# Performance work log

Measured on AMD Instinct MI355X. Metric: run time of the kernel, lower is better.

## Reference

```python
import jax, jax.numpy as jnp
import numpy as np

# Config (matches init_kwargs)
B, C, H, W = 32, 128, 12, 1200   # z: (B, in_dim, H, W)
DIN = C * H                       # 1536
FIX = 768                         # get_multiple(DIN // 2, 6)
OV = 4                            # overlap
G = 6                             # num_vqs
D = OV * FIX // G                 # 512 per-group embedding size (all equal)
K = 1024                          # codebook_size
COMMIT = 0.25


def setup_inputs() -> dict:
    key = jax.random.key(0)
    k1, k2, k3, k4 = jax.random.split(key, 4)
    z = jax.random.normal(k1, (B, C, H, W), dtype=jnp.float32)
    w_down = jax.random.normal(k2, (FIX, DIN), dtype=jnp.float32) * 0.02
    w_up = jax.random.normal(k3, (DIN, FIX), dtype=jnp.float32) * 0.02
    embedding = jax.random.normal(k4, (G, D, K), dtype=jnp.float32)  # per-group (embedding_size, num_embedding)
    return {"z": z, "w_down": w_down, "w_up": w_up, "embedding": embedding}


def _quantize_group(zg, emb):
    # zg: (B, T, D), emb: (D, K)
    zf = zg.reshape(-1, D)
    # squared euclidean distance: |z|^2 - 2 z@E + |E|^2 -> (N, K)
    dist = (zf * zf).sum(1, keepdims=True) - 2.0 * (zf @ emb) + (emb * emb).sum(0, keepdims=True)
    idx = jnp.argmin(dist, axis=1)            # (N,)
    q = jnp.take(emb.T, idx, axis=0).reshape(zg.shape)
    # straight-through estimator (training mode)
    zq = zg + jax.lax.stop_gradient(q - zg)
    loss = COMMIT * jnp.mean((jax.lax.stop_gradient(zq) - zg) ** 2)
    return zq, loss


def reference(z, w_down, w_up, embedding):
    # pre_process: (B,C,H,W) -> permute(0,2,3,1) -> permute(0,2,3,1) -> (B, W, C*H)
    x = jnp.transpose(z, (0, 3, 1, 2)).reshape(B, W, DIN)  # (B, W, C, H) flattened
    x = x @ w_down.T                                       # proj_down -> (B, W, FIX)
    T = W // OV
    x = x.reshape(B, T, OV * FIX)                          # (B, T, 3072)
    # split into G contiguous groups of size D along last axis -> (G, B, T, D)
    xg = jnp.transpose(x.reshape(B, T, G, D), (2, 0, 1, 3))
    zq_g, losses = jax.vmap(_quantize_group)(xg, embedding)
    vq_loss = losses.sum() / G
    # concat groups back -> (B, T, G*D)
    zq = jnp.transpose(zq_g, (1, 2, 0, 3)).reshape(B, T, G * D)
    # post_process: un-overlap, proj_up, back to (B, C, H, W)
    zq = zq.reshape(B, W, FIX)
    zq = zq @ w_up.T                                       # (B, W, DIN)
    zq = zq.reshape(B, W, C, H)
    zq = jnp.transpose(zq, (0, 3, 1, 2))                   # (B, H, W, C)
    zq = jnp.transpose(zq, (0, 3, 1, 2))                   # dim==4 -> (B, C, H, W)
    return zq, vq_loss
```

## Files before the change

kernel.cpp:

```cpp
#include <hip/hip_runtime.h>

#define BB 32
#define CC 128
#define HH 12
#define WW 1200
#define DIN 1536
#define FIXD 768
#define OVL 4
#define GG 6
#define DD 512
#define KK 1024
#define TT 300
#define NV 9600
#define MROWS 38400

#define Y_OFF     0
#define ET_OFF    29491200
#define NORM_OFF  32636928
#define BEST_OFF  32643072
#define LOSS_OFF  32758272
#define ZN_OFF    32758336
#define CNT_OFF   32873536
#define MAXN_OFF  32931136
#define LIST_OFF  32931200
#define YBF_OFF   36617600
#define EBF_OFF   51363200

#define BSWZ(c) ((c) + 4 * ((c) >> 5))

typedef __attribute__((ext_vector_type(8))) short bf16x8;
typedef __attribute__((ext_vector_type(4))) float f32x4;

static __device__ inline unsigned short f2bf(float x) {
    unsigned u = __float_as_uint(x);
    unsigned r = (u + 0x7fffu + ((u >> 16) & 1u)) >> 16;
    return (unsigned short)r;
}
static __device__ inline unsigned enc32(float s) {
    unsigned u = __float_as_uint(s);
    return (u & 0x80000000u) ? ~u : (u | 0x80000000u);
}

__global__ __launch_bounds__(256) void k_gemm_down(const float* __restrict__ z,
                                                   const float* __restrict__ w_down,
                                                   float* __restrict__ Y) {
    __shared__ float As[16][132];
    __shared__ float Bs[16][140];
    const int n0 = blockIdx.y * 128, f0 = blockIdx.x * 128;
    const int tid = threadIdx.x;
    const int arow = tid & 127;
    const int ak0 = tid >> 7;
    const int nA = n0 + arow;
    const int bA = nA / WW, wA = nA - bA * WW;
    const size_t zbase = (size_t)bA * (CC * HH * WW) + wA;
    const int bcol = tid >> 1, bq = tid & 1;
    const int bsc = BSWZ(bcol);
    const int trow = tid >> 4, tcol = tid & 15;
    const int bread = tcol * 8 + 4 * (tcol >> 2);
    float acc[8][8] = {};
    for (int kt = 0; kt < DIN; kt += 16) {
        #pragma unroll
        for (int i = 0; i < 8; i++) {
            const int kk = ak0 + i * 2;
            As[kk][arow] = z[zbase + (size_t)(kt + kk) * WW];
        }
        #pragma unroll
        for (int i = 0; i < 2; i++) {
            const int q = bq + i * 2;
            const float4 v = *(const float4*)&w_down[(size_t)(f0 + bcol) * DIN + kt + q * 4];
            Bs[q * 4 + 0][bsc] = v.x;
            Bs[q * 4 + 1][bsc] = v.y;
            Bs[q * 4 + 2][bsc] = v.z;
            Bs[q * 4 + 3][bsc] = v.w;
        }
        __syncthreads();
        #pragma unroll
        for (int k = 0; k < 16; k++) {
            float av[8], bv[8];
            *(float4*)&av[0] = *(const float4*)&As[k][trow * 8];
            *(float4*)&av[4] = *(const float4*)&As[k][trow * 8 + 4];
            *(float4*)&bv[0] = *(const float4*)&Bs[k][bread];
            *(float4*)&bv[4] = *(const float4*)&Bs[k][bread + 4];
            #pragma unroll
            for (int i = 0; i < 8; i++)
                #pragma unroll
                for (int j = 0; j < 8; j++)
                    acc[i][j] = fmaf(av[i], bv[j], acc[i][j]);
        }
        __syncthreads();
    }
    #pragma unroll
    for (int i = 0; i < 8; i++) {
        float4 o0, o1;
        o0.x = acc[i][0]; o0.y = acc[i][1]; o0.z = acc[i][2]; o0.w = acc[i][3];
        o1.x = acc[i][4]; o1.y = acc[i][5]; o1.z = acc[i][6]; o1.w = acc[i][7];
        float* yr = &Y[(size_t)(n0 + trow * 8 + i) * FIXD + f0 + tcol * 8];
        *(float4*)yr = o0;
        *(float4*)(yr + 4) = o1;
    }
}

__global__ __launch_bounds__(256) void k_transpose(const float* __restrict__ emb,
                                                   float* __restrict__ ET) {
    int i = blockIdx.x * 256 + threadIdx.x;
    if (i >= GG * KK * DD) return;
    int d = i & 511;
    int rem = i >> 9;
    int k = rem & 1023;
    int g = rem >> 10;
    ET[i] = emb[((g * DD + d) << 10) + k];
}

__global__ __launch_bounds__(64) void k_norms(const float* __restrict__ ET,
                                              float* __restrict__ norms,
                                              unsigned* __restrict__ maxnU) {
    const int code = blockIdx.x;
    const int lane = threadIdx.x;
    const float* row = ET + code * DD;
    double s = 0.0;
    #pragma unroll
    for (int r = 0; r < 8; r++) {
        float v = row[lane + r * 64];
        s += (double)v * (double)v;
    }
    #pragma unroll
    for (int off = 32; off; off >>= 1) s += __shfl_down(s, off);
    if (lane == 0) {
        const float nf = (float)s;
        norms[code] = nf;
        atomicMax(&maxnU[code >> 10], __float_as_uint(nf));
    }
}

__global__ __launch_bounds__(256) void k_ysplit(const float* __restrict__ Y,
                                                unsigned short* __restrict__ Ybf,
                                                float* __restrict__ znorm) {
    const int gv = blockIdx.x * 4 + (threadIdx.x >> 6);
    const int lane = threadIdx.x & 63;
    const int g = gv / NV, r = gv - g * NV;
    const int b = r / TT, t = r - b * TT;
    const int d0 = lane * 8;
    const int p = g * DD + d0;
    const int sg = p / FIXD, f = p - sg * FIXD;
    const float* yb = &Y[(size_t)((b * WW + t * OVL + sg) * FIXD + f)];
    const float4 y0 = *(const float4*)yb;
    const float4 y1 = *(const float4*)(yb + 4);
    unsigned short h[8];
    h[0] = f2bf(y0.x); h[1] = f2bf(y0.y); h[2] = f2bf(y0.z); h[3] = f2bf(y0.w);
    h[4] = f2bf(y1.x); h[5] = f2bf(y1.y); h[6] = f2bf(y1.z); h[7] = f2bf(y1.w);
    *(uint4*)&Ybf[(size_t)gv * DD + d0] = *(uint4*)&h[0];
    float s = 0.f;
    s = fmaf(y0.x, y0.x, s); s = fmaf(y0.y, y0.y, s);
    s = fmaf(y0.z, y0.z, s); s = fmaf(y0.w, y0.w, s);
    s = fmaf(y1.x, y1.x, s); s = fmaf(y1.y, y1.y, s);
    s = fmaf(y1.z, y1.z, s); s = fmaf(y1.w, y1.w, s);
    #pragma unroll
    for (int off = 32; off; off >>= 1) s += __shfl_down(s, off);
    if (lane == 0) znorm[gv] = s;
}

__global__ __launch_bounds__(256) void k_esplit(const float* __restrict__ ET,
                                                unsigned short* __restrict__ Ebf) {
    const size_t i8 = ((size_t)blockIdx.x * 256 + threadIdx.x) * 8;
    const float4 a = *(const float4*)&ET[i8];
    const float4 b = *(const float4*)&ET[i8 + 4];
    unsigned short h[8];
    h[0] = f2bf(a.x); h[1] = f2bf(a.y); h[2] = f2bf(a.z); h[3] = f2bf(a.w);
    h[4] = f2bf(b.x); h[5] = f2bf(b.y); h[6] = f2bf(b.z); h[7] = f2bf(b.w);
    *(uint4*)&Ebf[i8] = *(uint4*)&h[0];
}

__global__ __launch_bounds__(256) void k_dist4(const unsigned short* __restrict__ Ybf,
                                               const unsigned short* __restrict__ Ebf,
                                               const float* __restrict__ norms,
                                               const float* __restrict__ znorm,
                                               const unsigned* __restrict__ maxnU,
                                               unsigned* __restrict__ cnt,
                                               unsigned* __restrict__ list_) {
    __shared__ unsigned short Ah[128][40], Bh[128][40];
    __shared__ float margs[128];
    __shared__ unsigned redmin[128][2];
    __shared__ float thrs[128];
    const int ct = blockIdx.x;
    const int vt = blockIdx.y;
    const int g  = blockIdx.z;
    const int v0 = vt * 128, c0 = ct * 128;
    const int tid = threadIdx.x;
    const size_t ybase = ((size_t)g * NV + v0) * DD;
    const size_t ebase = ((size_t)g * KK + c0) * DD;
    const int srow = tid >> 1, sseg = (tid & 1) * 16;
    const int wv = tid >> 6, lane = tid & 63;
    const int wr = wv >> 1, wc = wv & 1;
    const int m0 = wr * 64, n0 = wc * 64;
    const int lr = lane & 15, lq = lane >> 4;

    if (tid < 128) {
        const int gv = g * NV + v0 + tid;
        margs[tid] = 0.032f * sqrtf(znorm[gv] * __uint_as_float(maxnU[g]));
    }

    f32x4 acc[4][4];
    #pragma unroll
    for (int i = 0; i < 4; i++)
        #pragma unroll
        for (int j = 0; j < 4; j++) acc[i][j] = (f32x4){0.f, 0.f, 0.f, 0.f};

    for (int kt = 0; kt < DD; kt += 32) {
        {
            const uint4 a0 = *(const uint4*)&Ybf[ybase + (size_t)srow * DD + kt + sseg];
            const uint4 a1 = *(const uint4*)&Ybf[ybase + (size_t)srow * DD + kt + sseg + 8];
            const uint4 b0 = *(const uint4*)&Ebf[ebase + (size_t)srow * DD + kt + sseg];
            const uint4 b1 = *(const uint4*)&Ebf[ebase + (size_t)srow * DD + kt + sseg + 8];
            *(uint4*)&Ah[srow][sseg]     = a0;
            *(uint4*)&Ah[srow][sseg + 8] = a1;
            *(uint4*)&Bh[srow][sseg]     = b0;
            *(uint4*)&Bh[srow][sseg + 8] = b1;
        }
        __syncthreads();
        bf16x8 ah[4], bh[4];
        #pragma unroll
        for (int i = 0; i < 4; i++) {
            ah[i] = *(bf16x8*)&Ah[m0 + i * 16 + lr][lq * 8];
            bh[i] = *(bf16x8*)&Bh[n0 + i * 16 + lr][lq * 8];
        }
        #pragma unroll
        for (int i = 0; i < 4; i++)
            #pragma unroll
            for (int j = 0; j < 4; j++)
                acc[i][j] = __builtin_amdgcn_mfma_f32_16x16x32_bf16(ah[i], bh[j], acc[i][j], 0, 0, 0);
        __syncthreads();
    }

    float nrmj[4];
    #pragma unroll
    for (int j = 0; j < 4; j++) nrmj[j] = norms[(g << 10) + c0 + n0 + j * 16 + lr];

    #pragma unroll
    for (int i = 0; i < 4; i++) {
        #pragma unroll
        for (int rr = 0; rr < 4; rr++) {
            unsigned kb = 0xFFFFFFFFu;
            #pragma unroll
            for (int j = 0; j < 4; j++) {
                const unsigned u = enc32(nrmj[j] - 2.0f * acc[i][j][rr]);
                kb = (u < kb) ? u : kb;
            }
            #pragma unroll
            for (int off = 1; off < 16; off <<= 1) {
                const unsigned o = __shfl_xor(kb, off);
                kb = (o < kb) ? o : kb;
            }
            if (lr == 0) redmin[m0 + i * 16 + lq * 4 + rr][wc] = kb;
        }
    }
    __syncthreads();
    if (tid < 128) {
        const unsigned a = redmin[tid][0], b = redmin[tid][1];
        const unsigned u = (a < b) ? a : b;
        const unsigned x = (u & 0x80000000u) ? (u & 0x7fffffffu) : ~u;
        thrs[tid] = __uint_as_float(x) + margs[tid];
    }
    __syncthreads();

    #pragma unroll
    for (int i = 0; i < 4; i++) {
        #pragma unroll
        for (int rr = 0; rr < 4; rr++) {
            const int row = m0 + i * 16 + lq * 4 + rr;
            const float thr = thrs[row];
            #pragma unroll
            for (int j = 0; j < 4; j++) {
                const float sc = nrmj[j] - 2.0f * acc[i][j][rr];
                if (sc <= thr) {
                    const int gv = g * NV + v0 + row;
                    const unsigned idx = atomicAdd(&cnt[gv], 1u);
                    if (idx < 64u)
                        list_[(size_t)gv * 64 + idx] = (unsigned)(c0 + n0 + j * 16 + lr);
                }
            }
        }
    }
}

__global__ __launch_bounds__(64) void k_rescore(const float* __restrict__ Y,
                                                const float* __restrict__ ET,
                                                const float* __restrict__ norms,
                                                const unsigned* __restrict__ cnt,
                                                const unsigned* __restrict__ list_,
                                                unsigned long long* __restrict__ best) {
    const int gv = blockIdx.x;
    const unsigned n = cnt[gv];
    if (n > 64u) return;
    const int lane = threadIdx.x;
    const int g = gv / NV, r = gv - g * NV;
    const int b = r / TT, t = r - b * TT;
    unsigned long long key = ~0ull;
    if (lane < (int)n) {
        const unsigned c = list_[(size_t)gv * 64 + lane];
        const float* erow = &ET[((size_t)((g << 10) + c)) * DD];
        float s = 0.f;
        for (int d4 = 0; d4 < 128; ++d4) {
            const int p = g * DD + d4 * 4;
            const int sg = p / FIXD, f = p - sg * FIXD;
            const float4 yv = *(const float4*)&Y[(size_t)((b * WW + t * OVL + sg) * FIXD + f)];
            const float4 ev = *(const float4*)&erow[d4 * 4];
            s = fmaf(yv.x, ev.x, s); s = fmaf(yv.y, ev.y, s);
            s = fmaf(yv.z, ev.z, s); s = fmaf(yv.w, ev.w, s);
        }
        const float sc = norms[(g << 10) + c] - 2.0f * s;
        key = ((unsigned long long)enc32(sc) << 32) | c;
    }
    #pragma unroll
    for (int off = 32; off; off >>= 1) {
        const unsigned long long o = __shfl_down(key, off);
        if (o < key) key = o;
    }
    if (lane == 0) best[gv] = key;
}

__global__ __launch_bounds__(256) void k_fallback(const float* __restrict__ Y,
                                                  const float* __restrict__ ET,
                                                  const float* __restrict__ norms,
                                                  const unsigned* __restrict__ cnt,
                                                  unsigned long long* __restrict__ best) {
    const int gv = blockIdx.x;
    if (cnt[gv] <= 64u) return;
    __shared__ float Yv[512];
    __shared__ unsigned long long red[256];
    const int tid = threadIdx.x;
    const int g = gv / NV, r = gv - g * NV;
    const int b = r / TT, t = r - b * TT;
    if (tid < 128) {
        const int p = g * DD + tid * 4;
        const int sg = p / FIXD, f = p - sg * FIXD;
        *(float4*)&Yv[tid * 4] = *(const float4*)&Y[(size_t)((b * WW + t * OVL + sg) * FIXD + f)];
    }
    __syncthreads();
    unsigned long long kb = ~0ull;
    for (int cc = 0; cc < 4; ++cc) {
        const int c = tid + cc * 256;
        const float* erow = &ET[((size_t)((g << 10) + c)) * DD];
        float s = 0.f;
        for (int d = 0; d < 512; ++d) s = fmaf(Yv[d], erow[d], s);
        const float sc = norms[(g << 10) + c] - 2.0f * s;
        const unsigned long long key = ((unsigned long long)enc32(sc) << 32) | (unsigned)c;
        if (key < kb) kb = key;
    }
    red[tid] = kb;
    __syncthreads();
    for (int off = 128; off; off >>= 1) {
        if (tid < off) { if (red[tid + off] < red[tid]) red[tid] = red[tid + off]; }
        __syncthreads();
    }
    if (tid == 0) best[gv] = red[0];
}

__global__ __launch_bounds__(256) void k_sumloss(const unsigned long long* __restrict__ best,
                                                 const float* __restrict__ znorm,
                                                 float* __restrict__ lossAcc) {
    const int v = blockIdx.x * 256 + threadIdx.x;
    const unsigned long long key = best[v];
    const unsigned u = (unsigned)(key >> 32);
    const unsigned x = (u & 0x80000000u) ? (u & 0x7fffffffu) : ~u;
    float s = __uint_as_float(x) + znorm[v];
    __shared__ float red[256];
    red[threadIdx.x] = s;
    __syncthreads();
    for (int off = 128; off; off >>= 1) {
        if (threadIdx.x < off) red[threadIdx.x] += red[threadIdx.x + off];
        __syncthreads();
    }
    if (threadIdx.x == 0) atomicAdd(lossAcc, red[0]);
}

__constant__ int SEG_G[8]  = {0, 1, 1, 2, 3, 4, 4, 5};
__constant__ int SEG_D0[8] = {0, 0, 256, 0, 0, 0, 256, 0};
__constant__ int SEG_L[8]  = {512, 256, 256, 512, 512, 256, 256, 512};
__constant__ int SEG_F0[8] = {0, 512, 0, 256, 0, 512, 0, 256};

__global__ __launch_bounds__(256) void k_table(const float* __restrict__ ET,
                                               const float* __restrict__ w_up,
                                               float* __restrict__ Tab) {
    __shared__ float As[16][68];
    __shared__ float Bs[16][140];
    const int bm = blockIdx.x;
    const int bn = blockIdx.y;
    const int seg = blockIdx.z;
    const int g = SEG_G[seg], d0 = SEG_D0[seg], len = SEG_L[seg], fb = SEG_F0[seg];
    const int tid = threadIdx.x;
    const int k0 = bm * 64, dout0 = bn * 128;
    const int arow = tid >> 2, aq = tid & 3;
    const int rbase = (tid >> 4) << 2;
    const int cgrp = tid & 15;
    const int bread = cgrp * 8 + 4 * (cgrp >> 2);
    const float* ETg = ET + (size_t)(g << 10) * DD;
    float acc[4][8] = {};
    for (int kt = 0; kt < len; kt += 16) {
        {
            const float4 v = *(const float4*)&ETg[(size_t)(k0 + arow) * DD + d0 + kt + aq * 4];
            As[aq * 4 + 0][arow] = v.x;
            As[aq * 4 + 1][arow] = v.y;
            As[aq * 4 + 2][arow] = v.z;
            As[aq * 4 + 3][arow] = v.w;
        }
        #pragma unroll
        for (int i = 0; i < 2; i++) {
            int fl = tid + i * 256;
            int col = fl >> 2, q = fl & 3;
            const int sc = BSWZ(col);
            const float4 v = *(const float4*)&w_up[(size_t)(dout0 + col) * FIXD + fb + kt + q * 4];
            Bs[q * 4 + 0][sc] = v.x;
            Bs[q * 4 + 1][sc] = v.y;
            Bs[q * 4 + 2][sc] = v.z;
            Bs[q * 4 + 3][sc] = v.w;
        }
        __syncthreads();
        #pragma unroll
        for (int k = 0; k < 16; k++) {
            const float4 a  = *(const float4*)&As[k][rbase];
            const float4 ba = *(const float4*)&Bs[k][bread];
            const float4 bb = *(const float4*)&Bs[k][bread + 4];
            const float av[4] = {a.x, a.y, a.z, a.w};
            const float bv[8] = {ba.x, ba.y, ba.z, ba.w, bb.x, bb.y, bb.z, bb.w};
            #pragma unroll
            for (int i = 0; i < 4; i++)
                #pragma unroll
                for (int j = 0; j < 8; j++)
                    acc[i][j] = fmaf(av[i], bv[j], acc[i][j]);
        }
        __syncthreads();
    }
    #pragma unroll
    for (int i = 0; i < 4; i++) {
        float4 o0, o1;
        o0.x = acc[i][0]; o0.y = acc[i][1]; o0.z = acc[i][2]; o0.w = acc[i][3];
        o1.x = acc[i][4]; o1.y = acc[i][5]; o1.z = acc[i][6]; o1.w = acc[i][7];
        float* tr = &Tab[(size_t)((seg << 10) + k0 + rbase + i) * DIN + dout0 + cgrp * 8];
        *(float4*)tr = o0;
        *(float4*)(tr + 4) = o1;
    }
}

__global__ __launch_bounds__(256) void k_scatter(const float* __restrict__ Tab,
                                                 const unsigned long long* __restrict__ best,
                                                 float* __restrict__ out) {
    __shared__ float Ls[64][65];
    const int dt = blockIdx.x;
    const int wt = blockIdx.y;
    const int b  = blockIdx.z;
    const int dout0 = dt * 64, w0 = wt * 64;
    const int wlim = (WW - w0 < 64) ? (WW - w0) : 64;
    const int tid = threadIdx.x;
    const int wi = tid >> 2, q = tid & 3;

    if (wi < wlim) {
        const int w = w0 + wi;
        const int s = w & 3;
        const int t = w >> 2;
        const int gEt[4] = {0, 1, 3, 4};
        const int gOt[4] = {1, 2, 4, 5};
        int ce = (int)(unsigned)best[gEt[s] * NV + b * TT + t];
        int co = (int)(unsigned)best[gOt[s] * NV + b * TT + t];
        size_t rowE = (size_t)(((2 * s) << 10) + ce) * DIN;
        size_t rowO = (size_t)(((2 * s + 1) << 10) + co) * DIN;
        #pragma unroll
        for (int rep = 0; rep < 4; rep++) {
            const int doff = rep * 16 + q * 4;
            const float4 a = *(const float4*)&Tab[rowE + dout0 + doff];
            const float4 c = *(const float4*)&Tab[rowO + dout0 + doff];
            Ls[wi][doff + 0] = a.x + c.x;
            Ls[wi][doff + 1] = a.y + c.y;
            Ls[wi][doff + 2] = a.z + c.z;
            Ls[wi][doff + 3] = a.w + c.w;
        }
    }
    __syncthreads();
    const size_t obase = (size_t)b * (CC * HH * WW) + (size_t)dout0 * WW + w0;
    #pragma unroll
    for (int i = 0; i < 16; i++) {
        int flat = tid + i * 256;
        int dr = flat >> 6, wj = flat & 63;
        if (wj < wlim) out[obase + (size_t)dr * WW + wj] = Ls[wj][dr];
    }
}

__global__ void k_finish(const float* __restrict__ lossAcc, float* __restrict__ out) {
    if (threadIdx.x == 0)
        out[58982400] = lossAcc[0] * (0.25f / 29491200.0f);
}

extern "C" void kernel_launch(void* const* d_in, const int* in_sizes, int n_in,
                              void* d_out, int out_size, void* d_ws, size_t ws_size,
                              hipStream_t stream) {
    const float* z      = (const float*)d_in[0];
    const float* w_down = (const float*)d_in[1];
    const float* w_up   = (const float*)d_in[2];
    const float* emb    = (const float*)d_in[3];
    float* out = (float*)d_out;

    float* ws    = (float*)d_ws;
    float* Y     = ws + Y_OFF;
    float* Tab   = ws + Y_OFF;
    float* ET    = ws + ET_OFF;
    float* norms = ws + NORM_OFF;
    unsigned long long* best = (unsigned long long*)(ws + BEST_OFF);
    float* lossA = ws + LOSS_OFF;
    float* znorm = ws + ZN_OFF;
    unsigned* cnt   = (unsigned*)(ws + CNT_OFF);
    unsigned* maxnU = (unsigned*)(ws + MAXN_OFF);
    unsigned* list_ = (unsigned*)(ws + LIST_OFF);
    unsigned short* Ybf = (unsigned short*)(ws + YBF_OFF);
    unsigned short* Ebf = (unsigned short*)(ws + EBF_OFF);

    hipMemsetAsync(cnt, 0, (size_t)GG * NV * sizeof(unsigned), stream);
    hipMemsetAsync(maxnU, 0, 64, stream);
    hipMemsetAsync(lossA, 0, sizeof(float), stream);

    dim3 gdown(6, 300);
    k_gemm_down<<<gdown, 256, 0, stream>>>(z, w_down, Y);

    k_transpose<<<(GG * KK * DD + 255) / 256, 256, 0, stream>>>(emb, ET);
    k_norms<<<GG * KK, 64, 0, stream>>>(ET, norms, maxnU);

    k_ysplit<<<GG * NV / 4, 256, 0, stream>>>(Y, Ybf, znorm);
    k_esplit<<<GG * KK * DD / (256 * 8), 256, 0, stream>>>(ET, Ebf);

    dim3 gdist(8, 75, GG);
    k_dist4<<<gdist, 256, 0, stream>>>(Ybf, Ebf, norms, znorm, maxnU, cnt, list_);

    k_rescore<<<GG * NV, 64, 0, stream>>>(Y, ET, norms, cnt, list_, best);
    k_fallback<<<GG * NV, 256, 0, stream>>>(Y, ET, norms, cnt, best);

    k_sumloss<<<225, 256, 0, stream>>>(best, znorm, lossA);

    dim3 gtab(16, 12, 8);
    k_table<<<gtab, 256, 0, stream>>>(ET, w_up, Tab);

    dim3 gsc(24, 19, 32);
    k_scatter<<<gsc, 256, 0, stream>>>(Tab, best, out);

    k_finish<<<1, 64, 0, stream>>>(lossA, out);
}
```

Baseline: 2.010 ms.

## Prune rescore candidates using global per-row bf16 minimum and merge fallback kernel

The distance kernel now records each row's global minimum approximate score via atomicMin and packs a truncated score into each candidate list entry. The rescore kernel filters candidates against a tighter global threshold before doing exact fp32 dot products. It also handles the rare overflow case inline, which replaces the separate fallback kernel launch. The goal is fewer exact rescoring dot products and fewer launches, at the cost of extra atomics and a threshold margin that must stay safe for correctness.

After: 2.155 ms. 1.07x slower.

```diff
diff --git a/kernel.cpp b/kernel.cpp
--- a/kernel.cpp
+++ b/kernel.cpp
@@ -20,6 +20,7 @@
 #define BEST_OFF  32643072
 #define LOSS_OFF  32758272
 #define ZN_OFF    32758336
+#define UMIN_OFF  32815936
 #define CNT_OFF   32873536
 #define MAXN_OFF  32931136
 #define LIST_OFF  32931200
@@ -39,6 +40,10 @@
 static __device__ inline unsigned enc32(float s) {
     unsigned u = __float_as_uint(s);
     return (u & 0x80000000u) ? ~u : (u | 0x80000000u);
+}
+static __device__ inline float dec32(unsigned u) {
+    const unsigned x = (u & 0x80000000u) ? (u & 0x7fffffffu) : ~u;
+    return __uint_as_float(x);
 }
 
 __global__ __launch_bounds__(256) void k_gemm_down(const float* __restrict__ z,
@@ -175,6 +180,7 @@
                                                const float* __restrict__ norms,
                                                const float* __restrict__ znorm,
                                                const unsigned* __restrict__ maxnU,
+                                               unsigned* __restrict__ umin,
                                                unsigned* __restrict__ cnt,
                                                unsigned* __restrict__ list_) {
     __shared__ unsigned short Ah[128][40], Bh[128][40];
@@ -257,8 +263,8 @@
     if (tid < 128) {
         const unsigned a = redmin[tid][0], b = redmin[tid][1];
         const unsigned u = (a < b) ? a : b;
-        const unsigned x = (u & 0x80000000u) ? (u & 0x7fffffffu) : ~u;
-        thrs[tid] = __uint_as_float(x) + margs[tid];
+        thrs[tid] = dec32(u) + margs[tid];
+        atomicMin(&umin[g * NV + v0 + tid], u);
     }
     __syncthreads();
 
@@ -274,41 +280,71 @@
                 if (sc <= thr) {
                     const int gv = g * NV + v0 + row;
                     const unsigned idx = atomicAdd(&cnt[gv], 1u);
-                    if (idx < 64u)
-                        list_[(size_t)gv * 64 + idx] = (unsigned)(c0 + n0 + j * 16 + lr);
+                    if (idx < 64u) {
+                        const unsigned entry = (enc32(sc) & 0xFFFFFC00u)
+                                             | (unsigned)(c0 + n0 + j * 16 + lr);
+                        list_[(size_t)gv * 64 + idx] = entry;
+                    }
                 }
             }
         }
     }
 }
 
-__global__ __launch_bounds__(64) void k_rescore(const float* __restrict__ Y,
-                                                const float* __restrict__ ET,
-                                                const float* __restrict__ norms,
-                                                const unsigned* __restrict__ cnt,
-                                                const unsigned* __restrict__ list_,
-                                                unsigned long long* __restrict__ best) {
-    const int gv = blockIdx.x;
-    const unsigned n = cnt[gv];
-    if (n > 64u) return;
-    const int lane = threadIdx.x;
+__global__ __launch_bounds__(256) void k_rescore2(const float* __restrict__ Y,
+                                                  const float* __restrict__ ET,
+                                                  const float* __restrict__ norms,
+                                                  const float* __restrict__ znorm,
+                                                  const unsigned* __restrict__ maxnU,
+                                                  const unsigned* __restrict__ umin,
+                                                  const unsigned* __restrict__ cnt,
+                                                  const unsigned* __restrict__ list_,
+                                                  unsigned long long* __restrict__ best) {
+    const int gv = blockIdx.x * 4 + (threadIdx.x >> 6);
+    const int lane = threadIdx.x & 63;
     const int g = gv / NV, r = gv - g * NV;
     const int b = r / TT, t = r - b * TT;
+    const unsigned n = cnt[gv];
+    const float thr = dec32(umin[gv])
+                    + 0.032f * sqrtf(znorm[gv] * __uint_as_float(maxnU[g]));
     unsigned long long key = ~0ull;
-    if (lane < (int)n) {
-        const unsigned c = list_[(size_t)gv * 64 + lane];
-        const float* erow = &ET[((size_t)((g << 10) + c)) * DD];
-        float s = 0.f;
-        for (int d4 = 0; d4 < 128; ++d4) {
-            const int p = g * DD + d4 * 4;
-            const int sg = p / FIXD, f = p - sg * FIXD;
-            const float4 yv = *(const float4*)&Y[(size_t)((b * WW + t * OVL + sg) * FIXD + f)];
-            const float4 ev = *(const float4*)&erow[d4 * 4];
-            s = fmaf(yv.x, ev.x, s); s = fmaf(yv.y, ev.y, s);
-            s = fmaf(yv.z, ev.z, s); s = fmaf(yv.w, ev.w, s);
-        }
-        const float sc = norms[(g << 10) + c] - 2.0f * s;
-        key = ((unsigned long long)enc32(sc) << 32) | c;
+    if (n <= 64u) {
+        unsigned c = 0xFFFFFFFFu;
+        if (lane < (int)n) {
+            const unsigned entry = list_[(size_t)gv * 64 + lane];
+            if (dec32(entry & 0xFFFFFC00u) <= thr) c = entry & 1023u;
+        }
+        if (c != 0xFFFFFFFFu) {
+            const float* erow = &ET[((size_t)((g << 10) + c)) * DD];
+            float s = 0.f;
+            for (int d4 = 0; d4 < 128; ++d4) {
+                const int p = g * DD + d4 * 4;
+                const int sg = p / FIXD, f = p - sg * FIXD;
+                const float4 yv = *(const float4*)&Y[(size_t)((b * WW + t * OVL + sg) * FIXD + f)];
+                const float4 ev = *(const float4*)&erow[d4 * 4];
+                s = fmaf(yv.x, ev.x, s); s = fmaf(yv.y, ev.y, s);
+                s = fmaf(yv.z, ev.z, s); s = fmaf(yv.w, ev.w, s);
+            }
+            const float sc = norms[(g << 10) + c] - 2.0f * s;
+            key = ((unsigned long long)enc32(sc) << 32) | c;
+        }
+    } else {
+        for (int cc = 0; cc < 16; ++cc) {
+            const unsigned c = (unsigned)(lane * 16 + cc);
+            const float* erow = &ET[((size_t)((g << 10) + c)) * DD];
+            float s = 0.f;
+            for (int d4 = 0; d4 < 128; ++d4) {
+                const int p = g * DD + d4 * 4;
+                const int sg = p / FIXD, f = p - sg * FIXD;
+                const float4 yv = *(const float4*)&Y[(size_t)((b * WW + t * OVL + sg) * FIXD + f)];
+                const float4 ev = *(const float4*)&erow[d4 * 4];
+                s = fmaf(yv.x, ev.x, s); s = fmaf(yv.y, ev.y, s);
+                s = fmaf(yv.z, ev.z, s); s = fmaf(yv.w, ev.w, s);
+            }
+            const float sc = norms[(g << 10) + c] - 2.0f * s;
+            const unsigned long long k2 = ((unsigned long long)enc32(sc) << 32) | c;
+            if (k2 < key) key = k2;
+        }
     }
     #pragma unroll
     for (int off = 32; off; off >>= 1) {
@@ -316,43 +352,6 @@
         if (o < key) key = o;
     }
     if (lane == 0) best[gv] = key;
-}
-
-__global__ __launch_bounds__(256) void k_fallback(const float* __restrict__ Y,
-                                                  const float* __restrict__ ET,
-                                                  const float* __restrict__ norms,
-                                                  const unsigned* __restrict__ cnt,
-                                                  unsigned long long* __restrict__ best) {
-    const int gv = blockIdx.x;
-    if (cnt[gv] <= 64u) return;
-    __shared__ float Yv[512];
-    __shared__ unsigned long long red[256];
-    const int tid = threadIdx.x;
-    const int g = gv / NV, r = gv - g * NV;
-    const int b = r / TT, t = r - b * TT;
-    if (tid < 128) {
-        const int p = g * DD + tid * 4;
-        const int sg = p / FIXD, f = p - sg * FIXD;
-        *(float4*)&Yv[tid * 4] = *(const float4*)&Y[(size_t)((b * WW + t * OVL + sg) * FIXD + f)];
-    }
-    __syncthreads();
-    unsigned long long kb = ~0ull;
-    for (int cc = 0; cc < 4; ++cc) {
-        const int c = tid + cc * 256;
-        const float* erow = &ET[((size_t)((g << 10) + c)) * DD];
-        float s = 0.f;
-        for (int d = 0; d < 512; ++d) s = fmaf(Yv[d], erow[d], s);
-        const float sc = norms[(g << 10) + c] - 2.0f * s;
-        const unsigned long long key = ((unsigned long long)enc32(sc) << 32) | (unsigned)c;
-        if (key < kb) kb = key;
-    }
-    red[tid] = kb;
-    __syncthreads();
-    for (int off = 128; off; off >>= 1) {
-        if (tid < off) { if (red[tid + off] < red[tid]) red[tid] = red[tid + off]; }
-        __syncthreads();
-    }
-    if (tid == 0) best[gv] = red[0];
 }
 
 __global__ __launch_bounds__(256) void k_sumloss(const unsigned long long* __restrict__ best,
@@ -360,9 +359,7 @@
                                                  float* __restrict__ lossAcc) {
     const int v = blockIdx.x * 256 + threadIdx.x;
     const unsigned long long key = best[v];
-    const unsigned u = (unsigned)(key >> 32);
-    const unsigned x = (u & 0x80000000u) ? (u & 0x7fffffffu) : ~u;
-    float s = __uint_as_float(x) + znorm[v];
+    float s = dec32((unsigned)(key >> 32)) + znorm[v];
     __shared__ float red[256];
     red[threadIdx.x] = s;
     __syncthreads();
@@ -459,8 +456,8 @@
         const int t = w >> 2;
         const int gEt[4] = {0, 1, 3, 4};
         const int gOt[4] = {1, 2, 4, 5};
-        int ce = (int)(unsigned)best[gEt[s] * NV + b * TT + t];
-        int co = (int)(unsigned)best[gOt[s] * NV + b * TT + t];
+        int ce = (int)((unsigned)best[gEt[s] * NV + b * TT + t] & 1023u);
+        int co = (int)((unsigned)best[gOt[s] * NV + b * TT + t] & 1023u);
         size_t rowE = (size_t)(((2 * s) << 10) + ce) * DIN;
         size_t rowO = (size_t)(((2 * s + 1) << 10) + co) * DIN;
         #pragma unroll
@@ -506,12 +503,14 @@
     unsigned long long* best = (unsigned long long*)(ws + BEST_OFF);
     float* lossA = ws + LOSS_OFF;
     float* znorm = ws + ZN_OFF;
+    unsigned* umin  = (unsigned*)(ws + UMIN_OFF);
     unsigned* cnt   = (unsigned*)(ws + CNT_OFF);
     unsigned* maxnU = (unsigned*)(ws + MAXN_OFF);
     unsigned* list_ = (unsigned*)(ws + LIST_OFF);
     unsigned short* Ybf = (unsigned short*)(ws + YBF_OFF);
     unsigned short* Ebf = (unsigned short*)(ws + EBF_OFF);
 
+    hipMemsetAsync(umin, 0xFF, (size_t)GG * NV * sizeof(unsigned), stream);
     hipMemsetAsync(cnt, 0, (size_t)GG * NV * sizeof(unsigned), stream);
     hipMemsetAsync(maxnU, 0, 64, stream);
     hipMemsetAsync(lossA, 0, sizeof(float), stream);
@@ -526,10 +525,9 @@
     k_esplit<<<GG * KK * DD / (256 * 8), 256, 0, stream>>>(ET, Ebf);
 
     dim3 gdist(8, 75, GG);
-    k_dist4<<<gdist, 256, 0, stream>>>(Ybf, Ebf, norms, znorm, maxnU, cnt, list_);
-
-    k_rescore<<<GG * NV, 64, 0, stream>>>(Y, ET, norms, cnt, list_, best);
-    k_fallback<<<GG * NV, 256, 0, stream>>>(Y, ET, norms, cnt, best);
+    k_dist4<<<gdist, 256, 0, stream>>>(Ybf, Ebf, norms, znorm, maxnU, umin, cnt, list_);
+
+    k_rescore2<<<GG * NV / 4, 256, 0, stream>>>(Y, ET, norms, znorm, maxnU, umin, cnt, list_, best);
 
     k_sumloss<<<225, 256, 0, stream>>>(best, znorm, lossA);
 
```
